# Kernel optimization log

Measured on AMD Instinct MI355X. Metric: run time of the kernel, lower is better.

The kernel has to match this reference:

```python
import jax, jax.numpy as jnp
import numpy as np

MAX_DIM = 1024
VOCAB = 257
DEPTH = 6
Q_DIM = MAX_DIM // 4  # 256
EXP_DIMS = [1, 2, 4, 8, 16, 32, 64, 128]  # expander sizes: current_q doubles up to Q_DIM
BATCH, SEQ = 8, 4096


def qlinear(q, W):
    """Quaternion Hamilton-product linear.
    q: [..., in, 4] (last dim = r,i,j,k components), W: [4, out, in] (stacked r,i,j,k weights).
    Returns [..., out, 4].
    """
    # P[..., o, w, a] = F.linear(component_a, W_w)  -> all 16 small GEMMs in one einsum
    P = jnp.einsum('...ia,woi->...owa', q, W)
    Pr, Pi, Pj, Pk = P[..., 0, :], P[..., 1, :], P[..., 2, :], P[..., 3, :]  # each [..., out, 4]
    out_r = Pr[..., 0] - Pi[..., 1] - Pj[..., 2] - Pk[..., 3]
    out_i = Pi[..., 0] + Pr[..., 1] + Pk[..., 2] - Pj[..., 3]
    out_j = Pj[..., 0] - Pk[..., 1] + Pr[..., 2] + Pi[..., 3]
    out_k = Pk[..., 0] + Pj[..., 1] - Pi[..., 2] + Pr[..., 3]
    return jnp.stack([out_r, out_i, out_j, out_k], axis=-1)


def qnormalize(q):
    norm = jnp.linalg.norm(q, axis=-1, keepdims=True)
    return q / (norm + 1e-8)


def setup_inputs() -> dict:
    key = jax.random.key(0)
    ks = jax.random.split(key, 4 + len(EXP_DIMS))
    inp = {}
    inp['x'] = jax.random.randint(ks[0], (BATCH, SEQ), 0, VOCAB)
    inp['emb'] = jax.random.normal(ks[1], (VOCAB, 4), dtype=jnp.float32)
    for idx, cq in enumerate(EXP_DIMS):
        scale = cq ** (-0.5)
        inp[f'w_exp{idx}'] = jax.random.uniform(ks[2 + idx], (4, cq, cq), jnp.float32, -scale, scale)
    scale = Q_DIM ** (-0.5)
    inp['w_layers'] = jax.random.uniform(ks[-2], (DEPTH, 4, Q_DIM, Q_DIM), jnp.float32, -scale, scale)
    inp['w_head'] = jax.random.normal(ks[-1], (VOCAB, MAX_DIM), dtype=jnp.float32) * MAX_DIM ** (-0.5)
    return inp


def reference(x, emb, w_exp0, w_exp1, w_exp2, w_exp3, w_exp4, w_exp5, w_exp6, w_exp7,
              w_layers, w_head):
    q = emb[x][:, :, None, :]  # [B, S, 1, 4]
    for w in (w_exp0, w_exp1, w_exp2, w_exp3, w_exp4, w_exp5, w_exp6, w_exp7):
        delta = jnp.tanh(qlinear(q, w))
        q = jnp.concatenate([q + delta, q - delta], axis=2)  # doubles quaternion dim
    for d in range(DEPTH):
        q = qnormalize(qlinear(q, w_layers[d]))
    stability_loss = jnp.mean(jnp.abs(q[..., 0]))
    h_flat = q.reshape(x.shape[0], x.shape[1], -1)  # [B, S, MAX_DIM]
    logits = jnp.einsum('bsd,vd->bsv', h_flat, w_head)
    return (logits, stability_loss)
```

## Files before the change

kernel.cpp:

```cpp
#include <hip/hip_runtime.h>


typedef _Float16 f16x8 __attribute__((ext_vector_type(8)));
typedef float    f32x4 __attribute__((ext_vector_type(4)));

#define GL2LDS16(gp, lp) __builtin_amdgcn_global_load_lds(                     \
    (const __attribute__((address_space(1))) void*)(gp),                       \
    (__attribute__((address_space(3))) void*)(lp), 16, 0, 0)

__device__ __forceinline__ unsigned short f2h(float f) {
  union { _Float16 h; unsigned short u; } c;
  c.h = (_Float16)f;
  return c.u;
}
__device__ __forceinline__ float h2f(unsigned short u) {
  union { unsigned short u; _Float16 h; } c;
  c.u = u;
  return (float)c.h;
}

__global__ __launch_bounds__(256) void expand_ham(
    const float* __restrict__ w, unsigned short* __restrict__ out,
    int cq, int kbits, int total) {
  int id = blockIdx.x * 256 + threadIdx.x;
  if (id >= total) return;
  const int K = 1 << kbits;
  const int n = id >> kbits;
  const int k = id & (K - 1);
  float val = 0.f;
  if (n < 4 * cq) {
    const int o = n >> 2, a = n & 3, i = k >> 2, b = k & 3;
    const int   comp[4][4] = {{0,1,2,3},{1,0,3,2},{2,3,0,1},{3,2,1,0}};
    const float sgn [4][4] = {{1.f,-1.f,-1.f,-1.f},{1.f,1.f,1.f,-1.f},
                              {1.f,-1.f,1.f,1.f},{1.f,1.f,-1.f,1.f}};
    val = sgn[a][b] * w[comp[a][b] * cq * cq + o * cq + i];
  }
  out[id] = f2h(val);
}

__global__ __launch_bounds__(256) void conv_head(
    const float* __restrict__ wh, unsigned short* __restrict__ out) {
  int id = blockIdx.x * 256 + threadIdx.x;
  int v = id >> 10, k = id & 1023;
  out[id] = f2h(v < 257 ? wh[v * 1024 + k] : 0.f);
}

template <int CQ>
__device__ __forceinline__ void exp_step(float (&q)[16][4],
                                         const float* __restrict__ w) {
  float d[CQ][4];
#pragma unroll
  for (int o = 0; o < CQ; o++) {
    float pr = 0.f, pi = 0.f, pj = 0.f, pk = 0.f;
#pragma unroll
    for (int i = 0; i < CQ; i++) {
      const float wr = w[0 * CQ * CQ + o * CQ + i];
      const float wi = w[1 * CQ * CQ + o * CQ + i];
      const float wj = w[2 * CQ * CQ + o * CQ + i];
      const float wk = w[3 * CQ * CQ + o * CQ + i];
      const float qr = q[i][0], qi = q[i][1], qj = q[i][2], qk = q[i][3];
      pr += wr * qr - wi * qi - wj * qj - wk * qk;
      pi += wi * qr + wr * qi + wk * qj - wj * qk;
      pj += wj * qr - wk * qi + wr * qj + wi * qk;
      pk += wk * qr + wj * qi - wi * qj + wr * qk;
    }
    d[o][0] = tanhf(pr); d[o][1] = tanhf(pi);
    d[o][2] = tanhf(pj); d[o][3] = tanhf(pk);
  }
#pragma unroll
  for (int o = 0; o < CQ; o++)
#pragma unroll
    for (int a = 0; a < 4; a++) {
      const float dd = d[o][a], qq = q[o][a];
      q[o][a]      = qq + dd;
      q[CQ + o][a] = qq - dd;
    }
}

__global__ __launch_bounds__(256) void embed_expand(
    const int* __restrict__ x, const float* __restrict__ emb,
    const float* __restrict__ w0, const float* __restrict__ w1,
    const float* __restrict__ w2, const float* __restrict__ w3,
    unsigned short* __restrict__ out) {
  const int t = blockIdx.x * 256 + threadIdx.x;
  float q[16][4];
  const int v = x[t];
  const float4 e = *(const float4*)(emb + v * 4);
  q[0][0] = e.x; q[0][1] = e.y; q[0][2] = e.z; q[0][3] = e.w;
  exp_step<1>(q, w0);
  exp_step<2>(q, w1);
  exp_step<4>(q, w2);
  exp_step<8>(q, w3);
  ushort4* o4 = (ushort4*)(out + (size_t)t * 64);
#pragma unroll
  for (int c = 0; c < 16; c++) {
    ushort4 u;
    u.x = f2h(q[c][0]); u.y = f2h(q[c][1]);
    u.z = f2h(q[c][2]); u.w = f2h(q[c][3]);
    o4[c] = u;
  }
}

template <int EPI>
__global__ __launch_bounds__(256) void gemm_epi(
    const unsigned short* __restrict__ W,
    const unsigned short* __restrict__ Act,
    unsigned short* __restrict__ OutB, float* __restrict__ OutF,
    int K, int Nreal, int ldout) {
  __shared__ unsigned short Wt[128 * 32];
  __shared__ unsigned short At[128 * 32];
  __shared__ float lsum[4];

  const int tid  = threadIdx.x;
  const int wave = tid >> 6;
  const int lane = tid & 63;
  const int l15  = lane & 15;
  const int quad = lane >> 4;
  const int mblock = blockIdx.x * 128;
  const int nblock = blockIdx.y * 128;
  const int wn = (wave & 1) * 64;
  const int wm = (wave >> 1) * 64;

  f32x4 acc[4][4];
  const f32x4 zero = {0.f, 0.f, 0.f, 0.f};
#pragma unroll
  for (int a = 0; a < 4; a++)
#pragma unroll
    for (int b = 0; b < 4; b++) acc[a][b] = zero;

  const int row0 = tid >> 2;
  const int sub  = tid & 3;
  const unsigned short* gW0 = W   + (size_t)(nblock + row0)      * K + sub * 8;
  const unsigned short* gW1 = W   + (size_t)(nblock + row0 + 64) * K + sub * 8;
  const unsigned short* gA0 = Act + (size_t)(mblock + row0)      * K + sub * 8;
  const unsigned short* gA1 = Act + (size_t)(mblock + row0 + 64) * K + sub * 8;
  unsigned short* lW0 = &Wt[(wave * 64) * 8];
  unsigned short* lW1 = &Wt[(256 + wave * 64) * 8];
  unsigned short* lA0 = &At[(wave * 64) * 8];
  unsigned short* lA1 = &At[(256 + wave * 64) * 8];

  for (int kb = 0; kb < K; kb += 32) {
    GL2LDS16(gW0 + kb, lW0);
    GL2LDS16(gW1 + kb, lW1);
    GL2LDS16(gA0 + kb, lA0);
    GL2LDS16(gA1 + kb, lA1);
    __syncthreads();

    f16x8 afr[4], bfr[4];
#pragma unroll
    for (int tn = 0; tn < 4; tn++)
      afr[tn] = *(const f16x8*)&Wt[(wn + tn * 16 + l15) * 32 + quad * 8];
#pragma unroll
    for (int tm = 0; tm < 4; tm++)
      bfr[tm] = *(const f16x8*)&At[(wm + tm * 16 + l15) * 32 + quad * 8];
#pragma unroll
    for (int tn = 0; tn < 4; tn++)
#pragma unroll
      for (int tm = 0; tm < 4; tm++)
        acc[tn][tm] = __builtin_amdgcn_mfma_f32_16x16x32_f16(
            afr[tn], bfr[tm], acc[tn][tm], 0, 0, 0);
    __syncthreads();
  }

  if constexpr (EPI == 0) {
#pragma unroll
    for (int tn = 0; tn < 4; tn++) {
      const int n = nblock + wn + tn * 16 + quad * 4;
      if (n < Nreal) {
#pragma unroll
        for (int tm = 0; tm < 4; tm++) {
          const int token = mblock + wm + tm * 16 + l15;
          const f32x4 v = acc[tn][tm];
          const unsigned short* ip = Act + (size_t)token * K + n;
          const float i0 = h2f(ip[0]), i1 = h2f(ip[1]);
          const float i2 = h2f(ip[2]), i3 = h2f(ip[3]);
          const float d0 = tanhf(v[0]), d1 = tanhf(v[1]);
          const float d2 = tanhf(v[2]), d3 = tanhf(v[3]);
          ushort4 up, um;
          up.x = f2h(i0 + d0); up.y = f2h(i1 + d1);
          up.z = f2h(i2 + d2); up.w = f2h(i3 + d3);
          um.x = f2h(i0 - d0); um.y = f2h(i1 - d1);
          um.z = f2h(i2 - d2); um.w = f2h(i3 - d3);
          *(ushort4*)&OutB[(size_t)token * ldout + n] = up;
          *(ushort4*)&OutB[(size_t)token * ldout + Nreal + n] = um;
        }
      }
    }
  } else if constexpr (EPI == 1 || EPI == 2) {
    float loss = 0.f;
#pragma unroll
    for (int tn = 0; tn < 4; tn++) {
      const int n = nblock + wn + tn * 16 + quad * 4;
#pragma unroll
      for (int tm = 0; tm < 4; tm++) {
        const int token = mblock + wm + tm * 16 + l15;
        const f32x4 v = acc[tn][tm];
        const float nrm =
            sqrtf(v[0] * v[0] + v[1] * v[1] + v[2] * v[2] + v[3] * v[3]);
        const float inv = 1.f / (nrm + 1e-8f);
        ushort4 u;
        u.x = f2h(v[0] * inv); u.y = f2h(v[1] * inv);
        u.z = f2h(v[2] * inv); u.w = f2h(v[3] * inv);
        *(ushort4*)&OutB[(size_t)token * ldout + n] = u;
        if constexpr (EPI == 2) loss += fabsf(v[0] * inv);
      }
    }
    if constexpr (EPI == 2) {
#pragma unroll
      for (int off = 32; off > 0; off >>= 1) loss += __shfl_down(loss, off);
      if (lane == 0) lsum[wave] = loss;
      __syncthreads();
      if (tid == 0)
        atomicAdd(OutF,
                  (lsum[0] + lsum[1] + lsum[2] + lsum[3]) * (1.f / 8388608.f));
    }
  } else {
#pragma unroll
    for (int tn = 0; tn < 4; tn++) {
      const int n = nblock + wn + tn * 16 + quad * 4;
      if (n < 257) {
#pragma unroll
        for (int tm = 0; tm < 4; tm++) {
          const int token = mblock + wm + tm * 16 + l15;
          const f32x4 v = acc[tn][tm];
#pragma unroll
          for (int r = 0; r < 4; r++)
            if (n + r < 257) OutF[(size_t)token * 257 + n + r] = v[r];
        }
      }
    }
  }
}

extern "C" void kernel_launch(void* const* d_in, const int* in_sizes, int n_in,
                              void* d_out, int out_size, void* d_ws,
                              size_t ws_size, hipStream_t stream) {
  const int*   x    = (const int*)d_in[0];
  const float* emb  = (const float*)d_in[1];
  const float* we0  = (const float*)d_in[2];
  const float* we1  = (const float*)d_in[3];
  const float* we2  = (const float*)d_in[4];
  const float* we3  = (const float*)d_in[5];
  const float* we4  = (const float*)d_in[6];
  const float* we5  = (const float*)d_in[7];
  const float* we6  = (const float*)d_in[8];
  const float* we7  = (const float*)d_in[9];
  const float* wlay = (const float*)d_in[10];
  const float* wh   = (const float*)d_in[11];
  float* out = (float*)d_out;

  char* p = (char*)d_ws;
  auto alloc = [&](size_t bytes) {
    void* r = (void*)p;
    p += (bytes + 255) & ~(size_t)255;
    return r;
  };
  unsigned short* act0 = (unsigned short*)alloc(32768ull * 1024 * 2);
  unsigned short* act1 = (unsigned short*)alloc(32768ull * 1024 * 2);
  unsigned short* E4 = (unsigned short*)alloc(128 * 64 * 2);
  unsigned short* E5 = (unsigned short*)alloc(128 * 128 * 2);
  unsigned short* E6 = (unsigned short*)alloc(256 * 256 * 2);
  unsigned short* E7 = (unsigned short*)alloc(512 * 512 * 2);
  unsigned short* EL = (unsigned short*)alloc(6ull * 1024 * 1024 * 2);
  unsigned short* WH = (unsigned short*)alloc(384 * 1024 * 2);

  hipMemsetAsync(out + 8421376, 0, 4, stream);

  expand_ham<<<dim3(8192 / 256), 256, 0, stream>>>(we4, E4, 16, 6, 128 * 64);
  expand_ham<<<dim3(16384 / 256), 256, 0, stream>>>(we5, E5, 32, 7, 128 * 128);
  expand_ham<<<dim3(65536 / 256), 256, 0, stream>>>(we6, E6, 64, 8, 256 * 256);
  expand_ham<<<dim3(262144 / 256), 256, 0, stream>>>(we7, E7, 128, 9,
                                                     512 * 512);
  for (int d = 0; d < 6; d++)
    expand_ham<<<dim3(1048576 / 256), 256, 0, stream>>>(
        wlay + (size_t)d * 262144, EL + (size_t)d * 1048576, 256, 10, 1048576);
  conv_head<<<dim3(384 * 1024 / 256), 256, 0, stream>>>(wh, WH);

  embed_expand<<<dim3(128), 256, 0, stream>>>(x, emb, we0, we1, we2, we3, act0);

  gemm_epi<0><<<dim3(256, 1), 256, 0, stream>>>(E4, act0, act1, nullptr, 64,
                                                64, 128);
  gemm_epi<0><<<dim3(256, 1), 256, 0, stream>>>(E5, act1, act0, nullptr, 128,
                                                128, 256);
  gemm_epi<0><<<dim3(256, 2), 256, 0, stream>>>(E6, act0, act1, nullptr, 256,
                                                256, 512);
  gemm_epi<0><<<dim3(256, 4), 256, 0, stream>>>(E7, act1, act0, nullptr, 512,
                                                512, 1024);

  unsigned short* a = act0;
  unsigned short* b = act1;
  for (int d = 0; d < 5; d++) {
    gemm_epi<1><<<dim3(256, 8), 256, 0, stream>>>(EL + (size_t)d * 1048576, a,
                                                  b, nullptr, 1024, 1024, 1024);
    unsigned short* t = a; a = b; b = t;
  }
  gemm_epi<2><<<dim3(256, 8), 256, 0, stream>>>(EL + 5ull * 1048576, a, b,
                                                out + 8421376, 1024, 1024,
                                                1024);
  { unsigned short* t = a; a = b; b = t; }

  gemm_epi<3><<<dim3(256, 3), 256, 0, stream>>>(WH, a, nullptr, out, 1024, 257,
                                                0);
}
```

Baseline: 982.5 us.

## Double-buffer GEMM K loop, load weights to registers, remap blocks, fuse prep kernels

```diff
diff --git a/kernel.cpp b/kernel.cpp
--- a/kernel.cpp
+++ b/kernel.cpp
@@ -19,11 +19,9 @@
   return (float)c.h;
 }
 
-__global__ __launch_bounds__(256) void expand_ham(
-    const float* __restrict__ w, unsigned short* __restrict__ out,
-    int cq, int kbits, int total) {
-  int id = blockIdx.x * 256 + threadIdx.x;
-  if (id >= total) return;
+__device__ __forceinline__ void expand_one(const float* __restrict__ w,
+                                           unsigned short* __restrict__ out,
+                                           int cq, int kbits, int id) {
   const int K = 1 << kbits;
   const int n = id >> kbits;
   const int k = id & (K - 1);
@@ -38,11 +36,33 @@
   out[id] = f2h(val);
 }
 
-__global__ __launch_bounds__(256) void conv_head(
-    const float* __restrict__ wh, unsigned short* __restrict__ out) {
-  int id = blockIdx.x * 256 + threadIdx.x;
-  int v = id >> 10, k = id & 1023;
-  out[id] = f2h(v < 257 ? wh[v * 1024 + k] : 0.f);
+__global__ __launch_bounds__(256) void prep_weights(
+    const float* __restrict__ we4, const float* __restrict__ we5,
+    const float* __restrict__ we6, const float* __restrict__ we7,
+    const float* __restrict__ wlay, const float* __restrict__ wh,
+    unsigned short* __restrict__ E4, unsigned short* __restrict__ E5,
+    unsigned short* __restrict__ E6, unsigned short* __restrict__ E7,
+    unsigned short* __restrict__ EL, unsigned short* __restrict__ WH) {
+  const int b = blockIdx.x;
+  const int tid = threadIdx.x;
+  if (b < 32) {
+    expand_one(we4, E4, 16, 6, b * 256 + tid);
+  } else if (b < 96) {
+    expand_one(we5, E5, 32, 7, (b - 32) * 256 + tid);
+  } else if (b < 352) {
+    expand_one(we6, E6, 64, 8, (b - 96) * 256 + tid);
+  } else if (b < 1376) {
+    expand_one(we7, E7, 128, 9, (b - 352) * 256 + tid);
+  } else if (b < 25952) {
+    const int d = (b - 1376) >> 12;
+    const int id = ((b - 1376) & 4095) * 256 + tid;
+    expand_one(wlay + (size_t)d * 262144, EL + (size_t)d * 1048576, 256, 10,
+               id);
+  } else {
+    const int id = (b - 25952) * 256 + tid;
+    const int v = id >> 10, k = id & 1023;
+    WH[id] = f2h(v < 257 ? wh[v * 1024 + k] : 0.f);
+  }
 }
 
 template <int CQ>
@@ -101,14 +121,13 @@
   }
 }
 
-template <int EPI>
+template <int EPI, int K>
 __global__ __launch_bounds__(256) void gemm_epi(
     const unsigned short* __restrict__ W,
     const unsigned short* __restrict__ Act,
     unsigned short* __restrict__ OutB, float* __restrict__ OutF,
-    int K, int Nreal, int ldout) {
-  __shared__ unsigned short Wt[128 * 32];
-  __shared__ unsigned short At[128 * 32];
+    int Nreal, int ldout) {
+  __shared__ unsigned short At[2][128 * 64];
   __shared__ float lsum[4];
 
   const int tid  = threadIdx.x;
@@ -116,8 +135,13 @@
   const int lane = tid & 63;
   const int l15  = lane & 15;
   const int quad = lane >> 4;
-  const int mblock = blockIdx.x * 128;
-  const int nblock = blockIdx.y * 128;
+
+  const int Gx = gridDim.x;
+  const int L  = blockIdx.y * Gx + blockIdx.x;
+  const int j  = L & 7;
+  const int s  = L >> 3;
+  const int nblock = (s % Gx) * 128;
+  const int mblock = (32 * j + s / Gx) * 128;
   const int wn = (wave & 1) * 64;
   const int wm = (wave >> 1) * 64;
 
@@ -130,36 +154,72 @@
 
   const int row0 = tid >> 2;
   const int sub  = tid & 3;
-  const unsigned short* gW0 = W   + (size_t)(nblock + row0)      * K + sub * 8;
-  const unsigned short* gW1 = W   + (size_t)(nblock + row0 + 64) * K + sub * 8;
   const unsigned short* gA0 = Act + (size_t)(mblock + row0)      * K + sub * 8;
   const unsigned short* gA1 = Act + (size_t)(mblock + row0 + 64) * K + sub * 8;
-  unsigned short* lW0 = &Wt[(wave * 64) * 8];
-  unsigned short* lW1 = &Wt[(256 + wave * 64) * 8];
-  unsigned short* lA0 = &At[(wave * 64) * 8];
-  unsigned short* lA1 = &At[(256 + wave * 64) * 8];
-
-  for (int kb = 0; kb < K; kb += 32) {
-    GL2LDS16(gW0 + kb, lW0);
-    GL2LDS16(gW1 + kb, lW1);
-    GL2LDS16(gA0 + kb, lA0);
-    GL2LDS16(gA1 + kb, lA1);
+
+  const unsigned short* gw[4];
+#pragma unroll
+  for (int tn = 0; tn < 4; tn++)
+    gw[tn] = W + (size_t)(nblock + wn + tn * 16 + l15) * K + quad * 8;
+
+  constexpr int NIT = K / 64;
+
+  GL2LDS16(gA0,      &At[0][wave * 512]);
+  GL2LDS16(gA1,      &At[0][2048 + wave * 512]);
+  GL2LDS16(gA0 + 32, &At[0][4096 + wave * 512]);
+  GL2LDS16(gA1 + 32, &At[0][4096 + 2048 + wave * 512]);
+  f16x8 wfrL[4], wfrH[4];
+#pragma unroll
+  for (int tn = 0; tn < 4; tn++) {
+    wfrL[tn] = *(const f16x8*)(gw[tn]);
+    wfrH[tn] = *(const f16x8*)(gw[tn] + 32);
+  }
+
+#pragma unroll
+  for (int it = 0; it < NIT; it++) {
+    const int kb = it * 64;
+    const int cur = it & 1, nxt = cur ^ 1;
     __syncthreads();
-
-    f16x8 afr[4], bfr[4];
-#pragma unroll
-    for (int tn = 0; tn < 4; tn++)
-      afr[tn] = *(const f16x8*)&Wt[(wn + tn * 16 + l15) * 32 + quad * 8];
-#pragma unroll
-    for (int tm = 0; tm < 4; tm++)
-      bfr[tm] = *(const f16x8*)&At[(wm + tm * 16 + l15) * 32 + quad * 8];
+    if (it + 1 < NIT) {
+      GL2LDS16(gA0 + kb + 64, &At[nxt][wave * 512]);
+      GL2LDS16(gA1 + kb + 64, &At[nxt][2048 + wave * 512]);
+      GL2LDS16(gA0 + kb + 96, &At[nxt][4096 + wave * 512]);
+      GL2LDS16(gA1 + kb + 96, &At[nxt][4096 + 2048 + wave * 512]);
+    }
+    f16x8 bfrL[4], bfrH[4];
+#pragma unroll
+    for (int tm = 0; tm < 4; tm++) {
+      bfrL[tm] = *(const f16x8*)&At[cur][(wm + tm * 16 + l15) * 32 + quad * 8];
+      bfrH[tm] =
+          *(const f16x8*)&At[cur][4096 + (wm + tm * 16 + l15) * 32 + quad * 8];
+    }
+    f16x8 wfrLn[4], wfrHn[4];
+    if (it + 1 < NIT) {
+#pragma unroll
+      for (int tn = 0; tn < 4; tn++) {
+        wfrLn[tn] = *(const f16x8*)(gw[tn] + kb + 64);
+        wfrHn[tn] = *(const f16x8*)(gw[tn] + kb + 96);
+      }
+    }
 #pragma unroll
     for (int tn = 0; tn < 4; tn++)
 #pragma unroll
       for (int tm = 0; tm < 4; tm++)
         acc[tn][tm] = __builtin_amdgcn_mfma_f32_16x16x32_f16(
-            afr[tn], bfr[tm], acc[tn][tm], 0, 0, 0);
-    __syncthreads();
+            wfrL[tn], bfrL[tm], acc[tn][tm], 0, 0, 0);
+#pragma unroll
+    for (int tn = 0; tn < 4; tn++)
+#pragma unroll
+      for (int tm = 0; tm < 4; tm++)
+        acc[tn][tm] = __builtin_amdgcn_mfma_f32_16x16x32_f16(
+            wfrH[tn], bfrH[tm], acc[tn][tm], 0, 0, 0);
+    if (it + 1 < NIT) {
+#pragma unroll
+      for (int tn = 0; tn < 4; tn++) {
+        wfrL[tn] = wfrLn[tn];
+        wfrH[tn] = wfrHn[tn];
+      }
+    }
   }
 
   if constexpr (EPI == 0) {
@@ -266,39 +326,31 @@
 
   hipMemsetAsync(out + 8421376, 0, 4, stream);
 
-  expand_ham<<<dim3(8192 / 256), 256, 0, stream>>>(we4, E4, 16, 6, 128 * 64);
-  expand_ham<<<dim3(16384 / 256), 256, 0, stream>>>(we5, E5, 32, 7, 128 * 128);
-  expand_ham<<<dim3(65536 / 256), 256, 0, stream>>>(we6, E6, 64, 8, 256 * 256);
-  expand_ham<<<dim3(262144 / 256), 256, 0, stream>>>(we7, E7, 128, 9,
-                                                     512 * 512);
-  for (int d = 0; d < 6; d++)
-    expand_ham<<<dim3(1048576 / 256), 256, 0, stream>>>(
-        wlay + (size_t)d * 262144, EL + (size_t)d * 1048576, 256, 10, 1048576);
-  conv_head<<<dim3(384 * 1024 / 256), 256, 0, stream>>>(wh, WH);
+  prep_weights<<<dim3(27488), 256, 0, stream>>>(we4, we5, we6, we7, wlay, wh,
+                                                E4, E5, E6, E7, EL, WH);
 
   embed_expand<<<dim3(128), 256, 0, stream>>>(x, emb, we0, we1, we2, we3, act0);
 
-  gemm_epi<0><<<dim3(256, 1), 256, 0, stream>>>(E4, act0, act1, nullptr, 64,
-                                                64, 128);
-  gemm_epi<0><<<dim3(256, 1), 256, 0, stream>>>(E5, act1, act0, nullptr, 128,
-                                                128, 256);
-  gemm_epi<0><<<dim3(256, 2), 256, 0, stream>>>(E6, act0, act1, nullptr, 256,
-                                                256, 512);
-  gemm_epi<0><<<dim3(256, 4), 256, 0, stream>>>(E7, act1, act0, nullptr, 512,
-                                                512, 1024);
+  gemm_epi<0, 64><<<dim3(1, 256), 256, 0, stream>>>(E4, act0, act1, nullptr,
+                                                    64, 128);
+  gemm_epi<0, 128><<<dim3(1, 256), 256, 0, stream>>>(E5, act1, act0, nullptr,
+                                                     128, 256);
+  gemm_epi<0, 256><<<dim3(2, 256), 256, 0, stream>>>(E6, act0, act1, nullptr,
+                                                     256, 512);
+  gemm_epi<0, 512><<<dim3(4, 256), 256, 0, stream>>>(E7, act1, act0, nullptr,
+                                                     512, 1024);
 
   unsigned short* a = act0;
   unsigned short* b = act1;
   for (int d = 0; d < 5; d++) {
-    gemm_epi<1><<<dim3(256, 8), 256, 0, stream>>>(EL + (size_t)d * 1048576, a,
-                                                  b, nullptr, 1024, 1024, 1024);
+    gemm_epi<1, 1024><<<dim3(8, 256), 256, 0, stream>>>(
+        EL + (size_t)d * 1048576, a, b, nullptr, 1024, 1024);
     unsigned short* t = a; a = b; b = t;
   }
-  gemm_epi<2><<<dim3(256, 8), 256, 0, stream>>>(EL + 5ull * 1048576, a, b,
-                                                out + 8421376, 1024, 1024,
-                                                1024);
+  gemm_epi<2, 1024><<<dim3(8, 256), 256, 0, stream>>>(
+      EL + 5ull * 1048576, a, b, out + 8421376, 1024, 1024);
   { unsigned short* t = a; a = b; b = t; }
 
-  gemm_epi<3><<<dim3(256, 3), 256, 0, stream>>>(WH, a, nullptr, out, 1024, 257,
-                                                0);
-}
+  gemm_epi<3, 1024><<<dim3(3, 256), 256, 0, stream>>>(WH, a, nullptr, out, 257,
+                                                      0);
+}
```

After: 1.452 ms. 47.8% more time.
